# Optimization experiments

Hardware: AMD Instinct MI355X
Metric: run time of the kernel (lower is better)

## Reference

```python
import jax, jax.numpy as jnp
import numpy as np
import math

C_CURV = 1.0          # manifold curvature c
KH = KW = 3
STRIDE = (1, 1)
PADDING = (1, 1)
DILATION = (1, 1)
IN_CH = 64            # includes time channel
OUT_CH = 64           # excludes time channel


def setup_inputs() -> dict:
    key = jax.random.key(0)
    k1, k2, k3 = jax.random.split(key, 3)
    B, H, W = 32, 64, 64
    x = jax.random.normal(k1, (B, H, W, IN_CH), dtype=jnp.float32)
    kk = KH * KW
    lin_in = (IN_CH - 1) * kk + 1  # 568
    stdv = math.sqrt(2.0 / ((IN_CH - 1) * kk))
    weight = jax.random.uniform(k2, (OUT_CH, lin_in), minval=-stdv, maxval=stdv, dtype=jnp.float32)
    bias = jax.random.uniform(k3, (OUT_CH,), minval=-stdv, maxval=stdv, dtype=jnp.float32)
    return {"x": x, "weight": weight, "bias": bias}


def _im2col(x):
    """x: [B,H,W,C] -> gathered patches [B,h_out,w_out,KH,KW,C] (torch Unfold semantics)."""
    B, H, W, C = x.shape
    xp = jnp.pad(x, ((0, 0), (PADDING[0], PADDING[0]), (PADDING[1], PADDING[1]), (0, 0)))
    h_out = (H + 2 * PADDING[0] - DILATION[0] * (KH - 1) - 1) // STRIDE[0] + 1
    w_out = (W + 2 * PADDING[1] - DILATION[1] * (KW - 1) - 1) // STRIDE[1] + 1
    rows = STRIDE[0] * jnp.arange(h_out)[:, None] + DILATION[0] * jnp.arange(KH)[None, :]  # [h_out,KH]
    cols = STRIDE[1] * jnp.arange(w_out)[:, None] + DILATION[1] * jnp.arange(KW)[None, :]  # [w_out,KW]
    g = xp[:, rows[:, None, :, None], cols[None, :, None, :], :]  # [B,h_out,w_out,KH,KW,C]
    return g, h_out, w_out


def reference(x, weight, bias):
    B = x.shape[0]
    kk = KH * KW
    g, h_out, w_out = _im2col(x)
    L = h_out * w_out
    # Time channel (channel 0) over kernel positions, clamped to sqrt(c)
    t = jnp.maximum(g[..., 0].reshape(B, L, kk), jnp.sqrt(jnp.float32(C_CURV)))
    t_rescaled = jnp.sqrt(jnp.sum(t * t, axis=-1, keepdims=True) - (kk - 1) * C_CURV)
    # Space channels in kernel-major, channel-minor order (matches torch reshape/transpose)
    s = g[..., 1:].reshape(B, L, kk * (IN_CH - 1))
    feat = jnp.concatenate([t_rescaled, s], axis=-1)  # [B, L, 568]
    # LorentzLinear: linear on features, recompute time from space norm
    y_space = jnp.einsum('blf,of->blo', feat, weight) + bias
    y_time = jnp.sqrt(jnp.sum(y_space * y_space, axis=-1, keepdims=True) + C_CURV)
    out = jnp.concatenate([y_time, y_space], axis=-1)
    return out.reshape(B, h_out, w_out, OUT_CH + 1)
```

## Files before the change

kernel.cpp:

```cpp
#include <hip/hip_runtime.h>
#include <cstdint>
#include <cstddef>

typedef __attribute__((ext_vector_type(8))) short short8v;
typedef __attribute__((ext_vector_type(4))) unsigned uint4v;
typedef __attribute__((ext_vector_type(4))) float floatx4;

#define LIN 568

__device__ __forceinline__ short f32_to_bf16(float f) {
  unsigned u = __builtin_bit_cast(unsigned, f);
  u += 0x7fffu + ((u >> 16) & 1u);
  return (short)(u >> 16);
}
__device__ __forceinline__ float bf16_to_f32(short s) {
  return __builtin_bit_cast(float, ((unsigned)(unsigned short)s) << 16);
}
__device__ __forceinline__ unsigned cvt_pk_bf16(float lo, float hi) {
  unsigned r;
  asm("v_cvt_pk_bf16_f32 %0, %1, %2" : "=v"(r) : "v"(lo), "v"(hi));
  return r;
}
template<int CTRL>
__device__ __forceinline__ float dpp_add(float v) {
  int y = __builtin_amdgcn_update_dpp(0, __builtin_bit_cast(int, v), CTRL, 0xF, 0xF, true);
  return v + __builtin_bit_cast(float, y);
}

__global__ void prep_weight(const float* __restrict__ w, short* __restrict__ wfragg) {
  int i = blockIdx.x * 256 + threadIdx.x;
  if (i >= 9 * 2 * 4 * 64 * 8) return;
  int j    = i & 7;
  int lane = (i >> 3) & 63;
  int nb   = (i >> 9) & 3;
  int half = (i >> 11) & 1;
  int tap  = i >> 12;
  int n = nb * 16 + (lane & 15);
  int c = half * 32 + ((lane >> 4) << 3) + j;
  float v = (c == 0) ? 0.0f : w[n * LIN + 1 + tap * 63 + (c - 1)];
  wfragg[i] = f32_to_bf16(v);
}

__launch_bounds__(256, 2)
__global__ void lconv_main(const float* __restrict__ x, const float* __restrict__ w,
                           const float* __restrict__ bias, const short* __restrict__ wfragg,
                           float* __restrict__ out) {
  __shared__ __align__(16) char shmem[4 * 4160 * 4];
  __shared__ float tres_s[4 * 64];
  short* xt = (short*)shmem;

  const int tid = threadIdx.x;
  const int bb = blockIdx.x >> 4;
  const int h0 = (blockIdx.x & 15) << 2;
  const float* xb = x + (size_t)bb * (64 * 64 * 64);

  const int lane = tid & 63;
  const int l15 = lane & 15;
  const int q = lane >> 4;
  const int wv = tid >> 6;

  float4 s0[12], s1[12];
#pragma unroll
  for (int i = 0; i < 12; ++i) {
    int idx = i * 256 + tid;
    int row = idx >> 9;
    int rem = idx & 511;
    int col = rem >> 3;
    int ch8 = (rem & 7) << 3;
    int h = h0 - 1 + row;
    s0[i] = {0.f, 0.f, 0.f, 0.f};
    s1[i] = {0.f, 0.f, 0.f, 0.f};
    if ((unsigned)h < 64u) {
      const float* p = xb + ((h * 64 + col) * 64 + ch8);
      s0[i] = *(const float4*)p;
      s1[i] = *(const float4*)(p + 4);
    }
  }

  const short* wfl = wfragg + lane * 8;
  short8v b0[4], b1[4], b2[4];
#pragma unroll
  for (int nb = 0; nb < 4; ++nb) {
    b0[nb] = *(const short8v*)(wfl + 0 * 2048 + nb * 512);
    b1[nb] = *(const short8v*)(wfl + 1 * 2048 + nb * 512);
    b2[nb] = *(const short8v*)(wfl + 2 * 2048 + nb * 512);
  }
  float bj[4], w0j[4];
#pragma unroll
  for (int nb = 0; nb < 4; ++nb) {
    int n = nb * 16 + l15;
    bj[nb] = bias[n];
    w0j[nb] = w[n * LIN];
  }

#pragma unroll
  for (int i = 0; i < 8; ++i) {
    int idx = i * 256 + tid;
    int row = idx >> 9;
    int rem = idx & 511;
    int col = rem >> 3;
    int ch8 = (rem & 7) << 3;
    uint4v o;
    o[0] = cvt_pk_bf16(s0[i].x, s0[i].y);
    o[1] = cvt_pk_bf16(s0[i].z, s0[i].w);
    o[2] = cvt_pk_bf16(s1[i].x, s1[i].y);
    o[3] = cvt_pk_bf16(s1[i].z, s1[i].w);
    *(uint4v*)&xt[(row * 66 + col + 1) * 72 + ch8] = o;
  }
  if (tid < 64) {
    int r = tid >> 4;
    int cc = (tid >> 3) & 1;
    int ch8 = (tid & 7) << 3;
    short8v z = {0, 0, 0, 0, 0, 0, 0, 0};
    *(short8v*)&xt[(r * 66 + cc * 65) * 72 + ch8] = z;
  }
  __syncthreads();

  floatx4 acc[4][4];
#pragma unroll
  for (int mb = 0; mb < 4; ++mb)
#pragma unroll
    for (int nb = 0; nb < 4; ++nb) acc[mb][nb] = floatx4{0.f, 0.f, 0.f, 0.f};

  auto do_step = [&](int step) {
    const int tap = step >> 1, half = step & 1;
    const int kh = tap / 3, kw = tap % 3;

    short8v bn[4];
    if (step + 3 < 18) {
#pragma unroll
      for (int nb = 0; nb < 4; ++nb)
        bn[nb] = *(const short8v*)(wfl + (step + 3) * 2048 + nb * 512);
    }

    const short* ab = &xt[((wv + kh) * 66 + kw + l15) * 72 + half * 32 + q * 8];
    short8v a[4];
#pragma unroll
    for (int mb = 0; mb < 4; ++mb)
      a[mb] = *(const short8v*)(ab + mb * 16 * 72);

#pragma unroll
    for (int mb = 0; mb < 4; ++mb) {
#pragma unroll
      for (int nb = 0; nb < 4; ++nb)
        acc[mb][nb] = __builtin_amdgcn_mfma_f32_16x16x32_bf16(a[mb], b0[nb], acc[mb][nb], 0, 0, 0);
    }
#pragma unroll
    for (int nb = 0; nb < 4; ++nb) { b0[nb] = b1[nb]; b1[nb] = b2[nb]; b2[nb] = bn[nb]; }
  };

#pragma unroll
  for (int step = 0; step < 6; ++step) do_step(step);

#pragma unroll
  for (int i = 8; i < 12; ++i) {
    int idx = i * 256 + tid;
    int row = idx >> 9;
    int rem = idx & 511;
    int col = rem >> 3;
    int ch8 = (rem & 7) << 3;
    uint4v o;
    o[0] = cvt_pk_bf16(s0[i].x, s0[i].y);
    o[1] = cvt_pk_bf16(s0[i].z, s0[i].w);
    o[2] = cvt_pk_bf16(s1[i].x, s1[i].y);
    o[3] = cvt_pk_bf16(s1[i].z, s1[i].w);
    *(uint4v*)&xt[(row * 66 + col + 1) * 72 + ch8] = o;
  }
  if (tid < 32) {
    int r = 4 + (tid >> 4);
    int cc = (tid >> 3) & 1;
    int ch8 = (tid & 7) << 3;
    short8v z = {0, 0, 0, 0, 0, 0, 0, 0};
    *(short8v*)&xt[(r * 66 + cc * 65) * 72 + ch8] = z;
  }
  __syncthreads();

#pragma unroll
  for (int step = 6; step < 18; ++step) do_step(step);

  {
    float ss = 0.f;
#pragma unroll
    for (int dh = 0; dh < 3; ++dh)
#pragma unroll
      for (int dw = 0; dw < 3; ++dw) {
        float tv = bf16_to_f32(xt[((wv + dh) * 66 + lane + dw) * 72]);
        tv = fmaxf(tv, 1.0f);
        ss += tv * tv;
      }
    tres_s[wv * 64 + lane] = sqrtf(ss - 8.0f);
  }

  __syncthreads();

  float* ostg = (float*)shmem + wv * 4160;
#pragma unroll
  for (int mb = 0; mb < 4; ++mb) {
    float4 t4 = *(const float4*)&tres_s[wv * 64 + mb * 16 + q * 4];
#pragma unroll
    for (int r = 0; r < 4; ++r) {
      int pcol = mb * 16 + q * 4 + r;
      float tr = t4[r];
      float v0 = acc[mb][0][r] + bj[0] + tr * w0j[0];
      float v1 = acc[mb][1][r] + bj[1] + tr * w0j[1];
      float v2 = acc[mb][2][r] + bj[2] + tr * w0j[2];
      float v3 = acc[mb][3][r] + bj[3] + tr * w0j[3];
      float ss = v0 * v0 + v1 * v1 + v2 * v2 + v3 * v3;
      ss = dpp_add<0xB1>(ss);
      ss = dpp_add<0x4E>(ss);
      ss = dpp_add<0x141>(ss);
      ss = dpp_add<0x140>(ss);
      float* pb = ostg + pcol * 65;
      if (l15 == 0) pb[0] = sqrtf(ss + 1.0f);
      pb[1 + l15]  = v0;
      pb[17 + l15] = v1;
      pb[33 + l15] = v2;
      pb[49 + l15] = v3;
    }
  }

  {
    float* orow = out + (size_t)((bb * 64 + h0 + wv) * 64) * 65;
#pragma unroll
    for (int it = 0; it < 16; ++it) {
      int off = it * 256 + lane * 4;
      *(float4*)(orow + off) = *(const float4*)(ostg + off);
    }
    if (lane < 16) {
      int off = 4096 + lane * 4;
      *(float4*)(orow + off) = *(const float4*)(ostg + off);
    }
  }
}

extern "C" void kernel_launch(void* const* d_in, const int* in_sizes, int n_in,
                              void* d_out, int out_size, void* d_ws, size_t ws_size,
                              hipStream_t stream) {
  const float* x = (const float*)d_in[0];
  const float* w = (const float*)d_in[1];
  const float* b = (const float*)d_in[2];
  float* out = (float*)d_out;
  short* wfragg = (short*)d_ws;

  prep_weight<<<144, 256, 0, stream>>>(w, wfragg);
  lconv_main<<<32 * 16, 256, 0, stream>>>(x, w, b, wfragg, out);
}
```

Before: 96.12 us.

## Split output channels across two waves per row using 512-thread blocks

Doubles the block to 512 threads so that each output row is handled by two waves. Each wave computes half of the 64 output channels, which halves its accumulator and weight-fragment registers and gives more waves per CU to hide load and MFMA latency. The per-pixel sum of squares for the time channel is now combined across the two waves through a small shared buffer, which costs an extra barrier. Input staging loads are also re-split into an early batch and a later batch around the first barrier.

```diff
diff --git a/kernel.cpp b/kernel.cpp
--- a/kernel.cpp
+++ b/kernel.cpp
@@ -41,12 +41,13 @@
   wfragg[i] = f32_to_bf16(v);
 }
 
-__launch_bounds__(256, 2)
+__launch_bounds__(512, 2)
 __global__ void lconv_main(const float* __restrict__ x, const float* __restrict__ w,
                            const float* __restrict__ bias, const short* __restrict__ wfragg,
                            float* __restrict__ out) {
   __shared__ __align__(16) char shmem[4 * 4160 * 4];
   __shared__ float tres_s[4 * 64];
+  __shared__ float pss[2][4][64];
   short* xt = (short*)shmem;
 
   const int tid = threadIdx.x;
@@ -58,11 +59,13 @@
   const int l15 = lane & 15;
   const int q = lane >> 4;
   const int wv = tid >> 6;
-
-  float4 s0[12], s1[12];
-#pragma unroll
-  for (int i = 0; i < 12; ++i) {
-    int idx = i * 256 + tid;
+  const int rr = wv >> 1;
+  const int nh = wv & 1;
+
+  float4 s0[6], s1[6];
+#pragma unroll
+  for (int i = 0; i < 4; ++i) {
+    int idx = i * 512 + tid;
     int row = idx >> 9;
     int rem = idx & 511;
     int col = rem >> 3;
@@ -78,24 +81,25 @@
   }
 
   const short* wfl = wfragg + lane * 8;
-  short8v b0[4], b1[4], b2[4];
-#pragma unroll
-  for (int nb = 0; nb < 4; ++nb) {
-    b0[nb] = *(const short8v*)(wfl + 0 * 2048 + nb * 512);
-    b1[nb] = *(const short8v*)(wfl + 1 * 2048 + nb * 512);
-    b2[nb] = *(const short8v*)(wfl + 2 * 2048 + nb * 512);
-  }
-  float bj[4], w0j[4];
-#pragma unroll
-  for (int nb = 0; nb < 4; ++nb) {
-    int n = nb * 16 + l15;
-    bj[nb] = bias[n];
-    w0j[nb] = w[n * LIN];
-  }
-
-#pragma unroll
-  for (int i = 0; i < 8; ++i) {
-    int idx = i * 256 + tid;
+  short8v b0[2], b1[2], b2[2];
+#pragma unroll
+  for (int nbl = 0; nbl < 2; ++nbl) {
+    const short* base = wfl + (nh * 2 + nbl) * 512;
+    b0[nbl] = *(const short8v*)(base + 0 * 2048);
+    b1[nbl] = *(const short8v*)(base + 1 * 2048);
+    b2[nbl] = *(const short8v*)(base + 2 * 2048);
+  }
+  float bj[2], w0j[2];
+#pragma unroll
+  for (int nbl = 0; nbl < 2; ++nbl) {
+    int n = (nh * 2 + nbl) * 16 + l15;
+    bj[nbl] = bias[n];
+    w0j[nbl] = w[n * LIN];
+  }
+
+#pragma unroll
+  for (int i = 0; i < 4; ++i) {
+    int idx = i * 512 + tid;
     int row = idx >> 9;
     int rem = idx & 511;
     int col = rem >> 3;
@@ -116,24 +120,41 @@
   }
   __syncthreads();
 
-  floatx4 acc[4][4];
+#pragma unroll
+  for (int i = 4; i < 6; ++i) {
+    int idx = i * 512 + tid;
+    int row = idx >> 9;
+    int rem = idx & 511;
+    int col = rem >> 3;
+    int ch8 = (rem & 7) << 3;
+    int h = h0 - 1 + row;
+    s0[i] = {0.f, 0.f, 0.f, 0.f};
+    s1[i] = {0.f, 0.f, 0.f, 0.f};
+    if ((unsigned)h < 64u) {
+      const float* p = xb + ((h * 64 + col) * 64 + ch8);
+      s0[i] = *(const float4*)p;
+      s1[i] = *(const float4*)(p + 4);
+    }
+  }
+
+  floatx4 acc[4][2];
 #pragma unroll
   for (int mb = 0; mb < 4; ++mb)
 #pragma unroll
-    for (int nb = 0; nb < 4; ++nb) acc[mb][nb] = floatx4{0.f, 0.f, 0.f, 0.f};
+    for (int nbl = 0; nbl < 2; ++nbl) acc[mb][nbl] = floatx4{0.f, 0.f, 0.f, 0.f};
 
   auto do_step = [&](int step) {
     const int tap = step >> 1, half = step & 1;
     const int kh = tap / 3, kw = tap % 3;
 
-    short8v bn[4];
+    short8v bn[2];
     if (step + 3 < 18) {
 #pragma unroll
-      for (int nb = 0; nb < 4; ++nb)
-        bn[nb] = *(const short8v*)(wfl + (step + 3) * 2048 + nb * 512);
-    }
-
-    const short* ab = &xt[((wv + kh) * 66 + kw + l15) * 72 + half * 32 + q * 8];
+      for (int nbl = 0; nbl < 2; ++nbl)
+        bn[nbl] = *(const short8v*)(wfl + (step + 3) * 2048 + (nh * 2 + nbl) * 512);
+    }
+
+    const short* ab = &xt[((rr + kh) * 66 + kw + l15) * 72 + half * 32 + q * 8];
     short8v a[4];
 #pragma unroll
     for (int mb = 0; mb < 4; ++mb)
@@ -142,19 +163,19 @@
 #pragma unroll
     for (int mb = 0; mb < 4; ++mb) {
 #pragma unroll
-      for (int nb = 0; nb < 4; ++nb)
-        acc[mb][nb] = __builtin_amdgcn_mfma_f32_16x16x32_bf16(a[mb], b0[nb], acc[mb][nb], 0, 0, 0);
-    }
-#pragma unroll
-    for (int nb = 0; nb < 4; ++nb) { b0[nb] = b1[nb]; b1[nb] = b2[nb]; b2[nb] = bn[nb]; }
+      for (int nbl = 0; nbl < 2; ++nbl)
+        acc[mb][nbl] = __builtin_amdgcn_mfma_f32_16x16x32_bf16(a[mb], b0[nbl], acc[mb][nbl], 0, 0, 0);
+    }
+#pragma unroll
+    for (int nbl = 0; nbl < 2; ++nbl) { b0[nbl] = b1[nbl]; b1[nbl] = b2[nbl]; b2[nbl] = bn[nbl]; }
   };
 
 #pragma unroll
   for (int step = 0; step < 6; ++step) do_step(step);
 
 #pragma unroll
-  for (int i = 8; i < 12; ++i) {
-    int idx = i * 256 + tid;
+  for (int i = 4; i < 6; ++i) {
+    int idx = i * 512 + tid;
     int row = idx >> 9;
     int rem = idx & 511;
     int col = rem >> 3;
@@ -184,51 +205,67 @@
     for (int dh = 0; dh < 3; ++dh)
 #pragma unroll
       for (int dw = 0; dw < 3; ++dw) {
-        float tv = bf16_to_f32(xt[((wv + dh) * 66 + lane + dw) * 72]);
+        float tv = bf16_to_f32(xt[((rr + dh) * 66 + lane + dw) * 72]);
         tv = fmaxf(tv, 1.0f);
         ss += tv * tv;
       }
-    tres_s[wv * 64 + lane] = sqrtf(ss - 8.0f);
-  }
-
-  __syncthreads();
-
-  float* ostg = (float*)shmem + wv * 4160;
+    tres_s[rr * 64 + lane] = sqrtf(ss - 8.0f);
+  }
+
 #pragma unroll
   for (int mb = 0; mb < 4; ++mb) {
-    float4 t4 = *(const float4*)&tres_s[wv * 64 + mb * 16 + q * 4];
+    float4 t4 = *(const float4*)&tres_s[rr * 64 + mb * 16 + q * 4];
 #pragma unroll
     for (int r = 0; r < 4; ++r) {
       int pcol = mb * 16 + q * 4 + r;
       float tr = t4[r];
       float v0 = acc[mb][0][r] + bj[0] + tr * w0j[0];
       float v1 = acc[mb][1][r] + bj[1] + tr * w0j[1];
-      float v2 = acc[mb][2][r] + bj[2] + tr * w0j[2];
-      float v3 = acc[mb][3][r] + bj[3] + tr * w0j[3];
-      float ss = v0 * v0 + v1 * v1 + v2 * v2 + v3 * v3;
+      acc[mb][0][r] = v0;
+      acc[mb][1][r] = v1;
+      float ss = v0 * v0 + v1 * v1;
       ss = dpp_add<0xB1>(ss);
       ss = dpp_add<0x4E>(ss);
       ss = dpp_add<0x141>(ss);
       ss = dpp_add<0x140>(ss);
+      if (l15 == 0) pss[nh][rr][pcol] = ss;
+    }
+  }
+
+  __syncthreads();
+
+  float* ostg = (float*)shmem + rr * 4160;
+#pragma unroll
+  for (int mb = 0; mb < 4; ++mb) {
+#pragma unroll
+    for (int r = 0; r < 4; ++r) {
+      int pcol = mb * 16 + q * 4 + r;
       float* pb = ostg + pcol * 65;
-      if (l15 == 0) pb[0] = sqrtf(ss + 1.0f);
-      pb[1 + l15]  = v0;
-      pb[17 + l15] = v1;
-      pb[33 + l15] = v2;
-      pb[49 + l15] = v3;
-    }
-  }
+      if (nh == 0) {
+        if (l15 == 0) pb[0] = sqrtf(pss[0][rr][pcol] + pss[1][rr][pcol] + 1.0f);
+        pb[1 + l15]  = acc[mb][0][r];
+        pb[17 + l15] = acc[mb][1][r];
+      } else {
+        pb[33 + l15] = acc[mb][0][r];
+        pb[49 + l15] = acc[mb][1][r];
+      }
+    }
+  }
+
+  __syncthreads();
 
   {
-    float* orow = out + (size_t)((bb * 64 + h0 + wv) * 64) * 65;
-#pragma unroll
-    for (int it = 0; it < 16; ++it) {
-      int off = it * 256 + lane * 4;
-      *(float4*)(orow + off) = *(const float4*)(ostg + off);
-    }
-    if (lane < 16) {
-      int off = 4096 + lane * 4;
-      *(float4*)(orow + off) = *(const float4*)(ostg + off);
+    float* orow = out + (size_t)((bb * 64 + h0 + rr) * 64) * 65;
+    const float* lrow = (const float*)shmem + rr * 4160;
+    int base = nh * 2080;
+#pragma unroll
+    for (int it = 0; it < 8; ++it) {
+      int off = base + it * 256 + lane * 4;
+      *(float4*)(orow + off) = *(const float4*)(lrow + off);
+    }
+    if (lane < 8) {
+      int off = base + 2048 + lane * 4;
+      *(float4*)(orow + off) = *(const float4*)(lrow + off);
     }
   }
 }
@@ -243,5 +280,5 @@
   short* wfragg = (short*)d_ws;
 
   prep_weight<<<144, 256, 0, stream>>>(w, wfragg);
-  lconv_main<<<32 * 16, 256, 0, stream>>>(x, w, b, wfragg, out);
-}
+  lconv_main<<<32 * 16, 512, 0, stream>>>(x, w, b, wfragg, out);
+}
```

Result: slower. 98.05 us (+2.0%).

## Drop register-staged input prefetch and roll tap loop to cut register pressure

Applied to the files above, without the earlier changes.

Input halo tiles are now loaded and converted straight into LDS in rolled groups of four, instead of being held in 96 registers and split around the first MFMA steps. The 18-step fully unrolled MFMA sequence becomes a rolled 9-tap loop with a two-deep weight-fragment prefetch. The weight buffer is padded with zero fragments so the prefetch can safely read past the last tap. The output copy loop is also rolled. The goal is lower VGPR use and smaller code, at the cost of no longer overlapping part of the global loads with compute.

```diff
diff --git a/kernel.cpp b/kernel.cpp
--- a/kernel.cpp
+++ b/kernel.cpp
@@ -29,7 +29,8 @@
 
 __global__ void prep_weight(const float* __restrict__ w, short* __restrict__ wfragg) {
   int i = blockIdx.x * 256 + threadIdx.x;
-  if (i >= 9 * 2 * 4 * 64 * 8) return;
+  if (i >= 20 * 2048) return;
+  if (i >= 9 * 2 * 4 * 64 * 8) { wfragg[i] = 0; return; }
   int j    = i & 7;
   int lane = (i >> 3) & 63;
   int nb   = (i >> 9) & 3;
@@ -59,61 +60,53 @@
   const int q = lane >> 4;
   const int wv = tid >> 6;
 
-  float4 s0[12], s1[12];
-#pragma unroll
-  for (int i = 0; i < 12; ++i) {
-    int idx = i * 256 + tid;
-    int row = idx >> 9;
-    int rem = idx & 511;
-    int col = rem >> 3;
-    int ch8 = (rem & 7) << 3;
-    int h = h0 - 1 + row;
-    s0[i] = {0.f, 0.f, 0.f, 0.f};
-    s1[i] = {0.f, 0.f, 0.f, 0.f};
-    if ((unsigned)h < 64u) {
-      const float* p = xb + ((h * 64 + col) * 64 + ch8);
-      s0[i] = *(const float4*)p;
-      s1[i] = *(const float4*)(p + 4);
-    }
-  }
-
-  const short* wfl = wfragg + lane * 8;
-  short8v b0[4], b1[4], b2[4];
-#pragma unroll
-  for (int nb = 0; nb < 4; ++nb) {
-    b0[nb] = *(const short8v*)(wfl + 0 * 2048 + nb * 512);
-    b1[nb] = *(const short8v*)(wfl + 1 * 2048 + nb * 512);
-    b2[nb] = *(const short8v*)(wfl + 2 * 2048 + nb * 512);
-  }
-  float bj[4], w0j[4];
-#pragma unroll
-  for (int nb = 0; nb < 4; ++nb) {
-    int n = nb * 16 + l15;
-    bj[nb] = bias[n];
-    w0j[nb] = w[n * LIN];
-  }
-
-#pragma unroll
-  for (int i = 0; i < 8; ++i) {
-    int idx = i * 256 + tid;
-    int row = idx >> 9;
-    int rem = idx & 511;
-    int col = rem >> 3;
-    int ch8 = (rem & 7) << 3;
-    uint4v o;
-    o[0] = cvt_pk_bf16(s0[i].x, s0[i].y);
-    o[1] = cvt_pk_bf16(s0[i].z, s0[i].w);
-    o[2] = cvt_pk_bf16(s1[i].x, s1[i].y);
-    o[3] = cvt_pk_bf16(s1[i].z, s1[i].w);
-    *(uint4v*)&xt[(row * 66 + col + 1) * 72 + ch8] = o;
-  }
-  if (tid < 64) {
+#pragma unroll 1
+  for (int g = 0; g < 3; ++g) {
+#pragma unroll
+    for (int k = 0; k < 4; ++k) {
+      int idx = (g * 4 + k) * 256 + tid;
+      int row = idx >> 9;
+      int rem = idx & 511;
+      int col = rem >> 3;
+      int ch8 = (rem & 7) << 3;
+      int h = h0 - 1 + row;
+      float4 v0 = {0.f, 0.f, 0.f, 0.f}, v1 = {0.f, 0.f, 0.f, 0.f};
+      if ((unsigned)h < 64u) {
+        const float* p = xb + ((h * 64 + col) * 64 + ch8);
+        v0 = *(const float4*)p;
+        v1 = *(const float4*)(p + 4);
+      }
+      uint4v o;
+      o[0] = cvt_pk_bf16(v0.x, v0.y);
+      o[1] = cvt_pk_bf16(v0.z, v0.w);
+      o[2] = cvt_pk_bf16(v1.x, v1.y);
+      o[3] = cvt_pk_bf16(v1.z, v1.w);
+      *(uint4v*)&xt[(row * 66 + col + 1) * 72 + ch8] = o;
+    }
+  }
+  if (tid < 96) {
     int r = tid >> 4;
     int cc = (tid >> 3) & 1;
     int ch8 = (tid & 7) << 3;
     short8v z = {0, 0, 0, 0, 0, 0, 0, 0};
     *(short8v*)&xt[(r * 66 + cc * 65) * 72 + ch8] = z;
   }
+
+  const short* wfl = wfragg + lane * 8;
+  short8v bA[4], bB[4];
+#pragma unroll
+  for (int nb = 0; nb < 4; ++nb) {
+    bA[nb] = *(const short8v*)(wfl + 0 * 2048 + nb * 512);
+    bB[nb] = *(const short8v*)(wfl + 1 * 2048 + nb * 512);
+  }
+  float bj[4], w0j[4];
+#pragma unroll
+  for (int nb = 0; nb < 4; ++nb) {
+    int n = nb * 16 + l15;
+    bj[nb] = bias[n];
+    w0j[nb] = w[n * LIN];
+  }
+
   __syncthreads();
 
   floatx4 acc[4][4];
@@ -122,61 +115,42 @@
 #pragma unroll
     for (int nb = 0; nb < 4; ++nb) acc[mb][nb] = floatx4{0.f, 0.f, 0.f, 0.f};
 
-  auto do_step = [&](int step) {
-    const int tap = step >> 1, half = step & 1;
-    const int kh = tap / 3, kw = tap % 3;
-
-    short8v bn[4];
-    if (step + 3 < 18) {
+#pragma unroll 1
+  for (int t = 0; t < 9; ++t) {
+    const int kh = (t * 11) >> 5;
+    const int kw = t - 3 * kh;
+    const short* ab = &xt[((wv + kh) * 66 + kw + l15) * 72 + q * 8];
+    const short8v z = {0, 0, 0, 0, 0, 0, 0, 0};
+
+    short8v a[4];
+#pragma unroll
+    for (int mb = 0; mb < 4; ++mb)
+      a[mb] = *(const short8v*)(ab + mb * 16 * 72);
+    if (kw == 0 && l15 == 0)  a[0] = z;
+    if (kw == 2 && l15 == 15) a[3] = z;
+#pragma unroll
+    for (int mb = 0; mb < 4; ++mb)
 #pragma unroll
       for (int nb = 0; nb < 4; ++nb)
-        bn[nb] = *(const short8v*)(wfl + (step + 3) * 2048 + nb * 512);
-    }
-
-    const short* ab = &xt[((wv + kh) * 66 + kw + l15) * 72 + half * 32 + q * 8];
-    short8v a[4];
-#pragma unroll
-    for (int mb = 0; mb < 4; ++mb)
-      a[mb] = *(const short8v*)(ab + mb * 16 * 72);
-
-#pragma unroll
-    for (int mb = 0; mb < 4; ++mb) {
+        acc[mb][nb] = __builtin_amdgcn_mfma_f32_16x16x32_bf16(a[mb], bA[nb], acc[mb][nb], 0, 0, 0);
+#pragma unroll
+    for (int nb = 0; nb < 4; ++nb)
+      bA[nb] = *(const short8v*)(wfl + (2 * t + 2) * 2048 + nb * 512);
+
+#pragma unroll
+    for (int mb = 0; mb < 4; ++mb)
+      a[mb] = *(const short8v*)(ab + 32 + mb * 16 * 72);
+    if (kw == 0 && l15 == 0)  a[0] = z;
+    if (kw == 2 && l15 == 15) a[3] = z;
+#pragma unroll
+    for (int mb = 0; mb < 4; ++mb)
 #pragma unroll
       for (int nb = 0; nb < 4; ++nb)
-        acc[mb][nb] = __builtin_amdgcn_mfma_f32_16x16x32_bf16(a[mb], b0[nb], acc[mb][nb], 0, 0, 0);
-    }
-#pragma unroll
-    for (int nb = 0; nb < 4; ++nb) { b0[nb] = b1[nb]; b1[nb] = b2[nb]; b2[nb] = bn[nb]; }
-  };
-
-#pragma unroll
-  for (int step = 0; step < 6; ++step) do_step(step);
-
-#pragma unroll
-  for (int i = 8; i < 12; ++i) {
-    int idx = i * 256 + tid;
-    int row = idx >> 9;
-    int rem = idx & 511;
-    int col = rem >> 3;
-    int ch8 = (rem & 7) << 3;
-    uint4v o;
-    o[0] = cvt_pk_bf16(s0[i].x, s0[i].y);
-    o[1] = cvt_pk_bf16(s0[i].z, s0[i].w);
-    o[2] = cvt_pk_bf16(s1[i].x, s1[i].y);
-    o[3] = cvt_pk_bf16(s1[i].z, s1[i].w);
-    *(uint4v*)&xt[(row * 66 + col + 1) * 72 + ch8] = o;
-  }
-  if (tid < 32) {
-    int r = 4 + (tid >> 4);
-    int cc = (tid >> 3) & 1;
-    int ch8 = (tid & 7) << 3;
-    short8v z = {0, 0, 0, 0, 0, 0, 0, 0};
-    *(short8v*)&xt[(r * 66 + cc * 65) * 72 + ch8] = z;
-  }
-  __syncthreads();
-
-#pragma unroll
-  for (int step = 6; step < 18; ++step) do_step(step);
+        acc[mb][nb] = __builtin_amdgcn_mfma_f32_16x16x32_bf16(a[mb], bB[nb], acc[mb][nb], 0, 0, 0);
+#pragma unroll
+    for (int nb = 0; nb < 4; ++nb)
+      bB[nb] = *(const short8v*)(wfl + (2 * t + 3) * 2048 + nb * 512);
+  }
 
   {
     float ss = 0.f;
@@ -221,7 +195,7 @@
 
   {
     float* orow = out + (size_t)((bb * 64 + h0 + wv) * 64) * 65;
-#pragma unroll
+#pragma unroll 1
     for (int it = 0; it < 16; ++it) {
       int off = it * 256 + lane * 4;
       *(float4*)(orow + off) = *(const float4*)(ostg + off);
@@ -242,6 +216,6 @@
   float* out = (float*)d_out;
   short* wfragg = (short*)d_ws;
 
-  prep_weight<<<144, 256, 0, stream>>>(w, wfragg);
+  prep_weight<<<160, 256, 0, stream>>>(w, wfragg);
   lconv_main<<<32 * 16, 256, 0, stream>>>(x, w, b, wfragg, out);
 }
```

Measured after the change: 98.08 us. +2.0%, slower.

## Stage weight fragments through LDS via async global_load_lds with triple buffering

Applied to the files above, without the earlier changes.

Weight B-fragments are no longer held in per-lane registers with a three-deep register pipeline. They are now loaded asynchronously into a 3-slot LDS ring with global_load_lds, using a vmcnt wait and a barrier at every step. All input rows are converted to LDS before the MMA loop instead of split around step 6, and edge A fragments are explicitly zeroed for kw==0 and kw==2. This lowers register pressure and shares weight loads across the workgroup, but adds a workgroup barrier per step and removes the overlap of the late input conversion with compute.

```diff
diff --git a/kernel.cpp b/kernel.cpp
--- a/kernel.cpp
+++ b/kernel.cpp
@@ -25,6 +25,11 @@
 __device__ __forceinline__ float dpp_add(float v) {
   int y = __builtin_amdgcn_update_dpp(0, __builtin_bit_cast(int, v), CTRL, 0xF, 0xF, true);
   return v + __builtin_bit_cast(float, y);
+}
+__device__ __forceinline__ void gload_lds16(const short* g, short* lds) {
+  __builtin_amdgcn_global_load_lds(
+      (const __attribute__((address_space(1))) void*)g,
+      (__attribute__((address_space(3))) void*)lds, 16, 0, 0);
 }
 
 __global__ void prep_weight(const float* __restrict__ w, short* __restrict__ wfragg) {
@@ -47,6 +52,7 @@
                            float* __restrict__ out) {
   __shared__ __align__(16) char shmem[4 * 4160 * 4];
   __shared__ float tres_s[4 * 64];
+  __shared__ short bstg[3 * 2048];
   short* xt = (short*)shmem;
 
   const int tid = threadIdx.x;
@@ -76,15 +82,6 @@
       s1[i] = *(const float4*)(p + 4);
     }
   }
-
-  const short* wfl = wfragg + lane * 8;
-  short8v b0[4], b1[4], b2[4];
-#pragma unroll
-  for (int nb = 0; nb < 4; ++nb) {
-    b0[nb] = *(const short8v*)(wfl + 0 * 2048 + nb * 512);
-    b1[nb] = *(const short8v*)(wfl + 1 * 2048 + nb * 512);
-    b2[nb] = *(const short8v*)(wfl + 2 * 2048 + nb * 512);
-  }
   float bj[4], w0j[4];
 #pragma unroll
   for (int nb = 0; nb < 4; ++nb) {
@@ -92,9 +89,8 @@
     bj[nb] = bias[n];
     w0j[nb] = w[n * LIN];
   }
-
-#pragma unroll
-  for (int i = 0; i < 8; ++i) {
+#pragma unroll
+  for (int i = 0; i < 12; ++i) {
     int idx = i * 256 + tid;
     int row = idx >> 9;
     int rem = idx & 511;
@@ -107,13 +103,17 @@
     o[3] = cvt_pk_bf16(s1[i].z, s1[i].w);
     *(uint4v*)&xt[(row * 66 + col + 1) * 72 + ch8] = o;
   }
-  if (tid < 64) {
+  if (tid < 96) {
     int r = tid >> 4;
     int cc = (tid >> 3) & 1;
     int ch8 = (tid & 7) << 3;
     short8v z = {0, 0, 0, 0, 0, 0, 0, 0};
     *(short8v*)&xt[(r * 66 + cc * 65) * 72 + ch8] = z;
   }
+
+  gload_lds16(wfragg + 0 * 2048 + tid * 8, &bstg[0 * 2048 + tid * 8]);
+  gload_lds16(wfragg + 1 * 2048 + tid * 8, &bstg[1 * 2048 + tid * 8]);
+
   __syncthreads();
 
   floatx4 acc[4][4];
@@ -123,60 +123,43 @@
     for (int nb = 0; nb < 4; ++nb) acc[mb][nb] = floatx4{0.f, 0.f, 0.f, 0.f};
 
   auto do_step = [&](int step) {
+    if (step < 17) asm volatile("s_waitcnt vmcnt(1)" ::: "memory");
+    else           asm volatile("s_waitcnt vmcnt(0)" ::: "memory");
+    __builtin_amdgcn_s_barrier();
+    __builtin_amdgcn_sched_barrier(0);
+
+    if (step + 2 < 18)
+      gload_lds16(wfragg + (step + 2) * 2048 + tid * 8,
+                  &bstg[((step + 2) % 3) * 2048 + tid * 8]);
+
     const int tap = step >> 1, half = step & 1;
     const int kh = tap / 3, kw = tap % 3;
 
-    short8v bn[4];
-    if (step + 3 < 18) {
-#pragma unroll
-      for (int nb = 0; nb < 4; ++nb)
-        bn[nb] = *(const short8v*)(wfl + (step + 3) * 2048 + nb * 512);
-    }
+    short8v b[4];
+    const short* bbp = &bstg[(step % 3) * 2048 + lane * 8];
+#pragma unroll
+    for (int nb = 0; nb < 4; ++nb)
+      b[nb] = *(const short8v*)(bbp + nb * 512);
 
     const short* ab = &xt[((wv + kh) * 66 + kw + l15) * 72 + half * 32 + q * 8];
     short8v a[4];
 #pragma unroll
     for (int mb = 0; mb < 4; ++mb)
       a[mb] = *(const short8v*)(ab + mb * 16 * 72);
+    short8v z = {0, 0, 0, 0, 0, 0, 0, 0};
+    if (kw == 0 && l15 == 0)  a[0] = z;
+    if (kw == 2 && l15 == 15) a[3] = z;
 
 #pragma unroll
     for (int mb = 0; mb < 4; ++mb) {
 #pragma unroll
       for (int nb = 0; nb < 4; ++nb)
-        acc[mb][nb] = __builtin_amdgcn_mfma_f32_16x16x32_bf16(a[mb], b0[nb], acc[mb][nb], 0, 0, 0);
-    }
-#pragma unroll
-    for (int nb = 0; nb < 4; ++nb) { b0[nb] = b1[nb]; b1[nb] = b2[nb]; b2[nb] = bn[nb]; }
+        acc[mb][nb] = __builtin_amdgcn_mfma_f32_16x16x32_bf16(a[mb], b[nb], acc[mb][nb], 0, 0, 0);
+    }
   };
 
 #pragma unroll
-  for (int step = 0; step < 6; ++step) do_step(step);
-
-#pragma unroll
-  for (int i = 8; i < 12; ++i) {
-    int idx = i * 256 + tid;
-    int row = idx >> 9;
-    int rem = idx & 511;
-    int col = rem >> 3;
-    int ch8 = (rem & 7) << 3;
-    uint4v o;
-    o[0] = cvt_pk_bf16(s0[i].x, s0[i].y);
-    o[1] = cvt_pk_bf16(s0[i].z, s0[i].w);
-    o[2] = cvt_pk_bf16(s1[i].x, s1[i].y);
-    o[3] = cvt_pk_bf16(s1[i].z, s1[i].w);
-    *(uint4v*)&xt[(row * 66 + col + 1) * 72 + ch8] = o;
-  }
-  if (tid < 32) {
-    int r = 4 + (tid >> 4);
-    int cc = (tid >> 3) & 1;
-    int ch8 = (tid & 7) << 3;
-    short8v z = {0, 0, 0, 0, 0, 0, 0, 0};
-    *(short8v*)&xt[(r * 66 + cc * 65) * 72 + ch8] = z;
-  }
-  __syncthreads();
-
-#pragma unroll
-  for (int step = 6; step < 18; ++step) do_step(step);
+  for (int step = 0; step < 18; ++step) do_step(step);
 
   {
     float ss = 0.f;
```

Result: no change. 97.95 us (+1.9%).
